# Performance work log

Measured on AMD Instinct MI355X. Metric: run time of the kernel, lower is better.

## Reference

```python
import jax, jax.numpy as jnp
import numpy as np
import math

B, T, XD, H, DD, P = 512, 256, 128, 512, 16, 32
IN = 2 * XD + DD  # GRUCell input size


def _init(key, shape, fan):
    stdv = 1.0 / math.sqrt(fan)
    return jax.random.uniform(key, shape, jnp.float32, -stdv, stdv)


def setup_inputs() -> dict:
    key = jax.random.key(0)
    ks = jax.random.split(key, 32)
    inp = {
        "values": jax.random.normal(ks[0], (B, T, XD), jnp.float32),
        "lens": jnp.full((B,), T, dtype=jnp.int32),  # lens[0] == max_len
        "static": jax.random.normal(ks[1], (B, DD), jnp.float32),
        "times": jax.random.uniform(ks[2], (B, T, XD), jnp.float32),
        "masks": (jax.random.uniform(ks[3], (B, T, XD)) < 0.8).astype(jnp.float32),
        "prototype": jax.random.normal(ks[4], (P, H), jnp.float32),
        "proto": True,
        # temp_decay_h: Linear(x_dim -> hidden), custom uniform(-1/sqrt(H), 1/sqrt(H))
        "Wd": _init(ks[5], (H, XD), H), "bd": _init(ks[6], (H,), XD),
        # hist_reg: Linear(hidden -> x_dim)
        "Wh": _init(ks[7], (XD, H), H), "bh": _init(ks[8], (XD,), H),
        "Wf": _init(ks[9], (XD, XD), XD), "bf": _init(ks[10], (XD,), XD),
        # ProtoAttn Q/K/V: Linear(hidden -> hidden)
        "Wq": _init(ks[11], (H, H), H), "bq": _init(ks[12], (H,), H),
        "Wk": _init(ks[13], (H, H), H), "bk": _init(ks[14], (H,), H),
        "Wv": _init(ks[15], (H, H), H), "bv": _init(ks[16], (H,), H),
        # gating W: Linear(2*hidden -> 1)
        "Wg": _init(ks[17], (1, 2 * H), 2 * H), "bg": _init(ks[18], (1,), 2 * H),
        # GRUCell
        "Wih": _init(ks[19], (3 * H, IN), H), "Whh": _init(ks[20], (3 * H, H), H),
        "bih": _init(ks[21], (3 * H,), H), "bhh": _init(ks[22], (3 * H,), H),
    }
    return inp


def _forward(values, static, times, masks, prototype,
             Wd, bd, Wh, bh, Wf, bf, Wq, bq, Wk, bk, Wv, bv, Wg, bg,
             Wih, Whh, bih, bhh, lens, proto):
    feat_m = 1.0 - jnp.eye(XD, dtype=values.dtype)  # zero-diagonal mask
    gamma = jnp.exp(-jax.nn.relu(jnp.einsum("btx,hx->bth", times, Wd) + bd))
    # attention key/value do not depend on h -> precompute
    keyp = prototype @ Wk.T + bk      # [P,H]
    valp = prototype @ Wv.T + bv      # [P,H]
    scale = 1.0 / math.sqrt(P)
    valid = (jnp.arange(T)[:, None] < lens[None, :]).astype(values.dtype)  # [T,B]

    xs = (jnp.swapaxes(values, 0, 1),  # [T,B,XD]
          jnp.swapaxes(masks, 0, 1),   # [T,B,XD]
          jnp.swapaxes(gamma, 0, 1),   # [T,B,H]
          valid[:, :, None])           # [T,B,1]

    h0 = jnp.zeros((B, H), values.dtype)
    xh0 = jnp.zeros((B, XD), values.dtype)

    def step(carry, xt):
        h, x_h = carry
        x, m, g, v = xt
        if proto:
            q = h @ Wq.T + bq                          # [B,H]
            score = (q @ keyp.T) * scale               # [B,P]
            attn = jax.nn.softmax(score, axis=-1)      # dropout omitted (eval)
            h1 = attn @ valp                           # [B,H]
            alpha = jax.nn.sigmoid(jnp.concatenate([h, h1], axis=1) @ Wg.T + bg)
            h = alpha * h + (1.0 - alpha) * h1
        h = h * g
        x_h = jnp.where(v > 0, h @ Wh.T + bh, x_h)
        x_c = m * x + (1.0 - m) * x_h
        z_h = x_c @ (Wf * feat_m).T + bf
        z_c = m * x + (1.0 - m) * z_h
        inp = jnp.concatenate([z_c, m, static], axis=1)
        gx = inp @ Wih.T + bih
        gh = h @ Whh.T + bhh
        xr, xz, xn = jnp.split(gx, 3, axis=1)
        hr, hz, hn = jnp.split(gh, 3, axis=1)
        r = jax.nn.sigmoid(xr + hr)
        z = jax.nn.sigmoid(xz + hz)
        n = jnp.tanh(xn + r * hn)
        h_new = (1.0 - z) * n + z * h
        h = jnp.where(v > 0, h_new, h)
        return (h, x_h), (h, x_c, z_c)

    (hN, _), (hs, x_cs, z_cs) = jax.lax.scan(step, (h0, xh0), xs)
    hs = jnp.swapaxes(hs, 0, 1)
    x_cs = jnp.swapaxes(x_cs, 0, 1)
    z_cs = jnp.swapaxes(z_cs, 0, 1)
    return hs, hN, x_cs, z_cs


def reference(values, lens, static, times, masks, prototype, proto,
              Wd, bd, Wh, bh, Wf, bf, Wq, bq, Wk, bk, Wv, bv, Wg, bg,
              Wih, Whh, bih, bhh):
    return _forward(values, static, times, masks, prototype,
                    Wd, bd, Wh, bh, Wf, bf, Wq, bq, Wk, bk, Wv, bv, Wg, bg,
                    Wih, Whh, bih, bhh, lens, bool(proto))
```

## Files before the change

kernel.cpp:

```cpp
#include <hip/hip_runtime.h>

#define NB 256
#define NT 1024

#define Bv 512
#define Tv 256
#define XDv 128
#define Hv 512
#define DDv 16
#define Pv 32

typedef short s8 __attribute__((ext_vector_type(8)));
typedef float f4 __attribute__((ext_vector_type(4)));
typedef unsigned long long u64;

#define OFF_KEYP 2048
#define OFF_VALP (OFF_KEYP + 16384)
#define OFF_MF   (OFF_VALP + 16384)
#define OFF_C    (OFF_MF + 16384)
#define OFF_VWG  (OFF_C + 32)
#define OFF_FRG  (OFF_VWG + 32)
#define US_WD   0
#define US_MS   65536
#define US_VP   81920
#define US_WH   98304
#define US_WF   163840
#define US_WHH  180224
#define US_WIH  966656
#define US_END  1409024
#define OFF_H   (OFF_FRG + (US_END/2))

#define OUT_HS  0
#define OUT_HN  (Bv*Tv*Hv)
#define OUT_XCS (OUT_HN + Bv*Hv)
#define OUT_ZCS (OUT_XCS + Bv*Tv*XDv)

struct Smem {
  unsigned short hA[32*520];
  unsigned short tA[32*136];
  unsigned short xcA[32*136];
  unsigned short inpA[32*296];
  unsigned short aA[32*40];
  unsigned short mA[32*136];
  unsigned short xhS[32*128];
  float xvS[32*132];
  float scS[32*34];
  float ghS[3*32*33];
  float gxS[3*32*33];
  float hp32[32*32];
  float al[32], rsm[32], cS[32], vwgS[32];
};

__device__ __forceinline__ unsigned short f2b(float f) {
  union { float f; unsigned int u; } x{f};
  unsigned int r = x.u + 0x7fffu + ((x.u >> 16) & 1u);
  return (unsigned short)(r >> 16);
}
__device__ __forceinline__ float b2f(unsigned short u) {
  union { unsigned int u; float f; } x{(unsigned int)u << 16};
  return x.f;
}
__device__ __forceinline__ float sig_f(float x) { return 1.f / (1.f + __expf(-x)); }
__device__ __forceinline__ float tanh_f(float x) {
  x = fminf(fmaxf(x, -15.f), 15.f);
  float e = __expf(2.f * x);
  return (e - 1.f) / (e + 1.f);
}
__device__ __forceinline__ s8 pack8(const float* p) {
  f4 a = *(const f4*)p; f4 b = *(const f4*)(p + 4);
  s8 r;
  r[0]=(short)f2b(a[0]); r[1]=(short)f2b(a[1]); r[2]=(short)f2b(a[2]); r[3]=(short)f2b(a[3]);
  r[4]=(short)f2b(b[0]); r[5]=(short)f2b(b[1]); r[6]=(short)f2b(b[2]); r[7]=(short)f2b(b[3]);
  return r;
}

__device__ __forceinline__ void gridbar(unsigned int* bar, unsigned int& lgen, int bid) {
  __syncthreads();
  if (threadIdx.x == 0) {
    __threadfence();
    const unsigned int target = ++lgen;
    unsigned int* grp = bar + (bid >> 4)*16;
    const unsigned int a =
        __hip_atomic_fetch_add(grp, 1u, __ATOMIC_ACQ_REL, __HIP_MEMORY_SCOPE_AGENT);
    if (a == 15u) {
      __hip_atomic_store(grp, 0u, __ATOMIC_RELAXED, __HIP_MEMORY_SCOPE_AGENT);
      const unsigned int r =
          __hip_atomic_fetch_add(bar + 384, 1u, __ATOMIC_ACQ_REL, __HIP_MEMORY_SCOPE_AGENT);
      if (r == 15u) {
        __hip_atomic_store(bar + 384, 0u, __ATOMIC_RELAXED, __HIP_MEMORY_SCOPE_AGENT);
        __hip_atomic_store(bar + 400, target, __ATOMIC_RELEASE, __HIP_MEMORY_SCOPE_AGENT);
      }
    }
    while (__hip_atomic_load(bar + 400, __ATOMIC_RELAXED, __HIP_MEMORY_SCOPE_AGENT) < target)
      __builtin_amdgcn_s_sleep(2);
    __threadfence();
  }
  __syncthreads();
}

__device__ __forceinline__ void rgbar_nf(unsigned int* bar, unsigned int& lgen, int rg) {
  __syncthreads();
  if (threadIdx.x == 0) {
    const unsigned int target = ++lgen;
    unsigned int* cnt = bar + 512 + rg*64;
    unsigned int* flg = cnt + 32;
    const unsigned int a =
        __hip_atomic_fetch_add(cnt, 1u, __ATOMIC_RELAXED, __HIP_MEMORY_SCOPE_AGENT);
    if (a == 15u) {
      __hip_atomic_store(cnt, 0u, __ATOMIC_RELAXED, __HIP_MEMORY_SCOPE_AGENT);
      asm volatile("s_waitcnt vmcnt(0)" ::: "memory");
      __hip_atomic_store(flg, target, __ATOMIC_RELAXED, __HIP_MEMORY_SCOPE_AGENT);
    } else {
      while (__hip_atomic_load(flg, __ATOMIC_RELAXED, __HIP_MEMORY_SCOPE_AGENT) < target)
        __builtin_amdgcn_s_sleep(2);
    }
  }
  __syncthreads();
}

#define SWZ(DST, NTILES, KT_, EXPR)                                            \
  { const int tot = (NTILES)*(KT_)*512;                                        \
    for (int f = gtid; f < tot; f += NB*NT) {                                  \
      const int e = f & 7, lane_ = (f >> 3) & 63, rem = f >> 9;                \
      const int kt = rem % (KT_), nt = rem / (KT_);                            \
      const int n = nt*16 + (lane_ & 15);                                      \
      const int k = kt*32 + ((lane_ >> 4) & 3)*8 + e;                          \
      (DST)[f] = f2b((EXPR));                                                  \
    } }

#define MFMA(a,b,c) __builtin_amdgcn_mfma_f32_16x16x32_bf16((a),(b),(c),0,0,0)
#define FRAG(P,idx) (*(const s8*)&(P)[((size_t)(idx))*8])
#define NTST(v,p) __builtin_nontemporal_store((v),(p))

__global__ __launch_bounds__(NT, 4)
void rits_main(const float* __restrict__ values, const int* __restrict__ lens,
               const float* __restrict__ statc, const float* __restrict__ times,
               const float* __restrict__ masks, const float* __restrict__ prototype,
               const int* __restrict__ protoflag,
               const float* __restrict__ Wd, const float* __restrict__ bd,
               const float* __restrict__ Wh, const float* __restrict__ bh,
               const float* __restrict__ Wf, const float* __restrict__ bf,
               const float* __restrict__ Wq, const float* __restrict__ bq,
               const float* __restrict__ Wk, const float* __restrict__ bk,
               const float* __restrict__ Wv, const float* __restrict__ bv,
               const float* __restrict__ Wg, const float* __restrict__ bg,
               const float* __restrict__ Wih, const float* __restrict__ Whh,
               const float* __restrict__ bih, const float* __restrict__ bhh,
               float* __restrict__ out, float* __restrict__ ws)
{
  const int bid = blockIdx.x, tid = threadIdx.x;
  const int gtid = bid*NT + tid;
  const int wv = tid >> 6, ln = tid & 63;
  const int l15 = ln & 15, l4 = ln >> 4;
  const int rg = (bid & 7)*2 + ((bid >> 7) & 1);
  const int cg = (bid >> 3) & 15;
  const int r0 = rg*32, c0 = cg*32;
  unsigned int* bar = (unsigned int*)ws;
  unsigned int lgenG = 0, lgenR = 0;
  unsigned short* frg = (unsigned short*)(ws + OFF_FRG);
  const unsigned short* wdW  = frg + US_WD;
  const unsigned short* msW  = frg + US_MS;
  const unsigned short* vpW  = frg + US_VP;
  const unsigned short* whW  = frg + US_WH;
  const unsigned short* wfW  = frg + US_WF;
  const unsigned short* whhW = frg + US_WHH;
  const unsigned short* wihW = frg + US_WIH;
  unsigned int* wsH = (unsigned int*)(ws + OFF_H);

  __shared__ Smem L;
  const bool proto = protoflag[0] != 0;
  const float scale = 0.17677669529663687f;

  for (int o = gtid; o < 2*Pv*Hv; o += NB*NT) {
    const int which = o >> 14, rem = o & 16383;
    const int p = rem >> 9, j = rem & 511;
    const float* W = which ? Wv : Wk;
    const float* bb = which ? bv : bk;
    const float* pr = prototype + p*Hv;
    const float* wr = W + j*Hv;
    float s = bb[j];
    #pragma unroll 4
    for (int k = 0; k < Hv; ++k) s += pr[k]*wr[k];
    ws[(which ? OFF_VALP : OFF_KEYP) + p*Hv + j] = s;
  }
  SWZ(frg + US_WD, 32, 4,  Wd[n*XDv + k])
  SWZ(frg + US_WH, 8, 16,  Wh[n*Hv + k])
  SWZ(frg + US_WF, 8, 4,   (n == k ? 0.f : Wf[n*XDv + k]))
  SWZ(frg + US_WHH, 96, 16,
      Whh[((size_t)(n >> 9)*Hv + (((n >> 5) & 15)*32 + ((n >> 4) & 1)*16 + (n & 15)))*Hv + k])
  SWZ(frg + US_WIH, 96, 9,
      (k < 272 ? Wih[((size_t)(n >> 9)*Hv + (((n >> 5) & 15)*32 + ((n >> 4) & 1)*16 + (n & 15)))*272 + k] : 0.f))
  gridbar(bar, lgenG, bid);

  {
    const float* keyp = ws + OFF_KEYP;
    const float* valp = ws + OFF_VALP;
    for (int o = gtid; o < Pv*Hv; o += NB*NT) {
      const int p = o >> 9, kc = o & 511;
      float s = 0.f;
      #pragma unroll 4
      for (int j = 0; j < Hv; ++j) s += keyp[p*Hv + j]*Wq[j*Hv + kc];
      ws[OFF_MF + o] = s;
    }
    if (gtid < 32) {
      float s = 0.f;
      for (int j = 0; j < Hv; ++j) s += bq[j]*keyp[gtid*Hv + j];
      ws[OFF_C + gtid] = s;
    } else if (gtid < 64) {
      const int p = gtid - 32;
      float s = 0.f;
      for (int j = 0; j < Hv; ++j) s += valp[p*Hv + j]*Wg[Hv + j];
      ws[OFF_VWG + p] = s;
    }
  }
  gridbar(bar, lgenG, bid);

  SWZ(frg + US_MS, 2, 16, (ws + OFF_MF)[n*Hv + k])
  SWZ(frg + US_VP, 32, 1, (ws + OFF_VALP)[k*Hv + n])
  gridbar(bar, lgenG, bid);

  for (int o = tid; o < 32*128; o += NT) L.xhS[o] = 0;
  if (tid < 32) { L.cS[tid] = ws[OFF_C + tid]; L.vwgS[tid] = ws[OFF_VWG + tid]; }
  for (int o = tid; o < 32*40; o += NT) {
    const int row = o / 40, cc = o % 40;
    L.inpA[row*296 + 256 + cc] =
        (cc < DDv) ? f2b(statc[(r0 + row)*DDv + cc]) : (unsigned short)0;
  }

  const int w8 = wv & 7;
  const int xcol8 = w8*16 + l15;
  const float bhR = bh[xcol8], bfR = bf[xcol8];
  int lensB2[8];
  #pragma unroll
  for (int rt = 0; rt < 2; ++rt)
    #pragma unroll
    for (int i = 0; i < 4; ++i)
      lensB2[rt*4 + i] = lens[r0 + rt*16 + l4*4 + i];
  float wgr[8];
  if (wv >= 8) {
    #pragma unroll
    for (int e = 0; e < 8; ++e) wgr[e] = Wg[ln*8 + e];
  }
  float bdW2[2];
  #pragma unroll
  for (int q = 0; q < 2; ++q) bdW2[q] = bd[(wv*2 + q)*16 + l15];
  const int crow = tid >> 5, cjj = tid & 31;
  float bihR[3], bhhR[3];
  #pragma unroll
  for (int g = 0; g < 3; ++g) { bihR[g] = bih[g*Hv + c0 + cjj]; bhhR[g] = bhh[g*Hv + c0 + cjj]; }
  const int lensG0 = lens[r0 + crow];
  const float bg0 = bg[0];

  float pv[4], pm[4], pt[4];
  #pragma unroll
  for (int i = 0; i < 4; ++i) {
    const int o = i*NT + tid, row = o >> 7, col = o & 127;
    const size_t a = ((size_t)(r0 + row)*Tv + 0)*XDv + col;
    pv[i] = values[a]; pm[i] = masks[a]; pt[i] = times[a];
  }
  __syncthreads();

  for (int t = 0; t < Tv; ++t) {
    if (t > 0) {
      const u64* src64 = (const u64*)(wsH + ((t - 1) & 1)*131072) + (size_t)r0*128;
      #pragma unroll
      for (int i = 0; i < 4; ++i) {
        const int o = i*NT + tid, row = o >> 7, cp = o & 127;
        ((u64*)&L.hA[row*520])[cp] = __hip_atomic_load(
            &src64[(size_t)row*128 + cp], __ATOMIC_RELAXED, __HIP_MEMORY_SCOPE_AGENT);
      }
    } else {
      for (int o = tid; o < 32*128; o += NT) {
        const int row = o >> 7, cp = o & 127;
        ((u64*)&L.hA[row*520])[cp] = 0ull;
      }
    }
    #pragma unroll
    for (int i = 0; i < 4; ++i) {
      const int o = i*NT + tid, row = o >> 7, col = o & 127;
      L.xvS[row*132 + col] = pv[i];
      L.mA[row*136 + col]  = f2b(pm[i]);
      L.tA[row*136 + col]  = f2b(pt[i]);
    }
    {
      const int tn = (t + 1 < Tv) ? t + 1 : t;
      #pragma unroll
      for (int i = 0; i < 4; ++i) {
        const int o = i*NT + tid, row = o >> 7, col = o & 127;
        const size_t a = ((size_t)(r0 + row)*Tv + tn)*XDv + col;
        pv[i] = values[a]; pm[i] = masks[a]; pt[i] = times[a];
      }
    }
    __syncthreads();

    if (proto) {
      if (wv < 2) {
        const int nt = wv;
        f4 acc0 = {0.f,0.f,0.f,0.f}, acc1 = {0.f,0.f,0.f,0.f};
        #pragma unroll
        for (int kt = 0; kt < 16; ++kt) {
          s8 b  = FRAG(msW, (nt*16 + kt)*64 + ln);
          s8 a0 = *(const s8*)&L.hA[(l15)*520 + kt*32 + l4*8];
          s8 a1 = *(const s8*)&L.hA[(16 + l15)*520 + kt*32 + l4*8];
          acc0 = MFMA(a0, b, acc0);
          acc1 = MFMA(a1, b, acc1);
        }
        #pragma unroll
        for (int i = 0; i < 4; ++i) {
          L.scS[(l4*4 + i)*34 + nt*16 + l15]        = acc0[i];
          L.scS[(16 + l4*4 + i)*34 + nt*16 + l15]   = acc1[i];
        }
      } else if (wv >= 8) {
        #pragma unroll
        for (int rr = 0; rr < 4; ++rr) {
          const int row = (wv - 8)*4 + rr;
          s8 hv8 = *(const s8*)&L.hA[row*520 + ln*8];
          float s = 0.f;
          #pragma unroll
          for (int e = 0; e < 8; ++e) s += b2f((unsigned short)hv8[e]) * wgr[e];
          s += __shfl_xor(s, 1);  s += __shfl_xor(s, 2);  s += __shfl_xor(s, 4);
          s += __shfl_xor(s, 8);  s += __shfl_xor(s, 16); s += __shfl_xor(s, 32);
          if (ln == 0) L.scS[row*34 + 32] = s;
        }
      }
    }
    __syncthreads();

    if (proto) {
      const int row = wv*2 + (ln >> 5);
      const int p = ln & 31;
      const float sc = (L.scS[row*34 + p] + L.cS[p]) * scale;
      float mx = sc;
      mx = fmaxf(mx, __shfl_xor(mx, 1));  mx = fmaxf(mx, __shfl_xor(mx, 2));
      mx = fmaxf(mx, __shfl_xor(mx, 4));  mx = fmaxf(mx, __shfl_xor(mx, 8));
      mx = fmaxf(mx, __shfl_xor(mx, 16));
      const float e = __expf(sc - mx);
      float sm = e;
      sm += __shfl_xor(sm, 1); sm += __shfl_xor(sm, 2); sm += __shfl_xor(sm, 4);
      sm += __shfl_xor(sm, 8); sm += __shfl_xor(sm, 16);
      float a1 = e * L.vwgS[p];
      a1 += __shfl_xor(a1, 1); a1 += __shfl_xor(a1, 2); a1 += __shfl_xor(a1, 4);
      a1 += __shfl_xor(a1, 8); a1 += __shfl_xor(a1, 16);
      L.aA[row*40 + p] = f2b(e);
      if (p == 0) {
        L.rsm[row] = 1.f / sm;
        L.al[row] = sig_f(L.scS[row*34 + 32] + a1 / sm + bg0);
      }
    }
    __syncthreads();

    {
      s8 ta[2][4]; s8 aa[2];
      #pragma unroll
      for (int rt = 0; rt < 2; ++rt) {
        #pragma unroll
        for (int kt = 0; kt < 4; ++kt)
          ta[rt][kt] = *(const s8*)&L.tA[(rt*16 + l15)*136 + kt*32 + l4*8];
        if (proto) aa[rt] = *(const s8*)&L.aA[(rt*16 + l15)*40 + l4*8];
      }
      #pragma unroll
      for (int q = 0; q < 2; ++q) {
        const int nt = wv*2 + q;
        const int col = nt*16 + l15;
        f4 g2[2] = {{0.f,0.f,0.f,0.f},{0.f,0.f,0.f,0.f}};
        f4 h12[2] = {{0.f,0.f,0.f,0.f},{0.f,0.f,0.f,0.f}};
        #pragma unroll
        for (int kt = 0; kt < 4; ++kt) {
          s8 b = FRAG(wdW, (nt*4 + kt)*64 + ln);
          g2[0] = MFMA(ta[0][kt], b, g2[0]);
          g2[1] = MFMA(ta[1][kt], b, g2[1]);
        }
        if (proto) {
          s8 b = FRAG(vpW, nt*64 + ln);
          h12[0] = MFMA(aa[0], b, h12[0]);
          h12[1] = MFMA(aa[1], b, h12[1]);
        }
        #pragma unroll
        for (int rt = 0; rt < 2; ++rt) {
          #pragma unroll
          for (int i = 0; i < 4; ++i) {
            const int row = rt*16 + l4*4 + i;
            const float gam = __expf(-fmaxf(g2[rt][i] + bdW2[q], 0.f));
            const float hbf = b2f(L.hA[row*520 + col]);
            float hp;
            if (proto) {
              const float av = L.al[row];
              hp = (av*hbf + (1.f - av)*h12[rt][i]*L.rsm[row]) * gam;
            } else hp = hbf * gam;
            L.hA[row*520 + col] = f2b(hp);
            const unsigned cc = (unsigned)(col - c0);
            if (cc < 32u) L.hp32[row*32 + cc] = hp;
          }
        }
      }
    }
    __syncthreads();

    if (wv < 8) {
      f4 accX[2] = {{0.f,0.f,0.f,0.f},{0.f,0.f,0.f,0.f}};
      #pragma unroll
      for (int kt = 0; kt < 16; ++kt) {
        s8 b  = FRAG(whW, (wv*16 + kt)*64 + ln);
        s8 a0 = *(const s8*)&L.hA[(l15)*520 + kt*32 + l4*8];
        s8 a1 = *(const s8*)&L.hA[(16 + l15)*520 + kt*32 + l4*8];
        accX[0] = MFMA(a0, b, accX[0]);
        accX[1] = MFMA(a1, b, accX[1]);
      }
      #pragma unroll
      for (int rt = 0; rt < 2; ++rt) {
        #pragma unroll
        for (int i = 0; i < 4; ++i) {
          const int row = rt*16 + l4*4 + i;
          const int b = r0 + row;
          float xh = accX[rt][i] + bhR;
          if (t < lensB2[rt*4 + i]) L.xhS[row*128 + xcol8] = f2b(xh);
          else                      xh = b2f(L.xhS[row*128 + xcol8]);
          const float xv = L.xvS[row*132 + xcol8], mv = b2f(L.mA[row*136 + xcol8]);
          const float xc = mv*xv + (1.f - mv)*xh;
          if (cg == 0) NTST(xc, &out[OUT_XCS + ((size_t)b*Tv + t)*XDv + xcol8]);
          L.xcA[row*136 + xcol8] = f2b(xc);
        }
      }
    } else if (wv < 14) {
      const int j = wv - 8, g = j >> 1, hf = j & 1;
      const int ntG = g*32 + cg*2 + hf;
      const int cLoc = hf*16 + l15;
      f4 accG[2] = {{0.f,0.f,0.f,0.f},{0.f,0.f,0.f,0.f}};
      #pragma unroll
      for (int kt = 0; kt < 16; ++kt) {
        s8 b  = FRAG(whhW, (ntG*16 + kt)*64 + ln);
        s8 a0 = *(const s8*)&L.hA[(l15)*520 + kt*32 + l4*8];
        s8 a1 = *(const s8*)&L.hA[(16 + l15)*520 + kt*32 + l4*8];
        accG[0] = MFMA(a0, b, accG[0]);
        accG[1] = MFMA(a1, b, accG[1]);
      }
      #pragma unroll
      for (int rt = 0; rt < 2; ++rt)
        #pragma unroll
        for (int i = 0; i < 4; ++i)
          L.ghS[g*1056 + (rt*16 + l4*4 + i)*33 + cLoc] = accG[rt][i];
    }
    __syncthreads();

    {
      const int wrt = wv >> 3;
      f4 acc = {0.f,0.f,0.f,0.f};
      #pragma unroll
      for (int kt = 0; kt < 4; ++kt) {
        s8 a = *(const s8*)&L.xcA[(wrt*16 + l15)*136 + kt*32 + l4*8];
        acc = MFMA(a, FRAG(wfW, (w8*4 + kt)*64 + ln), acc);
      }
      #pragma unroll
      for (int i = 0; i < 4; ++i) {
        const int row = wrt*16 + l4*4 + i;
        const float xv = L.xvS[row*132 + xcol8], mv = b2f(L.mA[row*136 + xcol8]);
        const float zc = mv*xv + (1.f - mv)*(acc[i] + bfR);
        if (cg == 0) NTST(zc, &out[OUT_ZCS + ((size_t)(r0 + row)*Tv + t)*XDv + xcol8]);
        L.inpA[row*296 + xcol8]       = f2b(zc);
        L.inpA[row*296 + 128 + xcol8] = f2b(mv);
      }
    }
    __syncthreads();

    if (wv < 12) {
      const int g = wv >> 2, sub = wv & 3;
      const int hf = sub >> 1, rt = sub & 1;
      const int ntG = g*32 + cg*2 + hf;
      const int cLoc = hf*16 + l15;
      f4 acc = {0.f,0.f,0.f,0.f};
      #pragma unroll
      for (int kt = 0; kt < 9; ++kt) {
        s8 a = *(const s8*)&L.inpA[(rt*16 + l15)*296 + kt*32 + l4*8];
        acc = MFMA(a, FRAG(wihW, (ntG*9 + kt)*64 + ln), acc);
      }
      #pragma unroll
      for (int i = 0; i < 4; ++i)
        L.gxS[g*1056 + (rt*16 + l4*4 + i)*33 + cLoc] = acc[i];
    }
    __syncthreads();

    unsigned int* dst = wsH + (t & 1)*131072;
    {
      const int row = crow;
      const int b = r0 + row, jc = c0 + cjj;
      const float xr = L.gxS[row*33 + cjj]        + bihR[0];
      const float xz = L.gxS[1056 + row*33 + cjj] + bihR[1];
      const float xn = L.gxS[2112 + row*33 + cjj] + bihR[2];
      const float hr = L.ghS[row*33 + cjj]        + bhhR[0];
      const float hz = L.ghS[1056 + row*33 + cjj] + bhhR[1];
      const float hn = L.ghS[2112 + row*33 + cjj] + bhhR[2];
      const float r = sig_f(xr + hr), z = sig_f(xz + hz);
      const float n = tanh_f(xn + r*hn);
      const float hpv = L.hp32[row*32 + cjj];
      const float hfv = (t < lensG0) ? ((1.f - z)*n + z*hpv) : hpv;
      NTST(hfv, &out[OUT_HS + ((size_t)b*Tv + t)*Hv + jc]);
      if (t == Tv - 1) NTST(hfv, &out[OUT_HN + (size_t)b*Hv + jc]);
      const float partner = __shfl_xor(hfv, 1);
      if ((cjj & 1) == 0) {
        const unsigned int pk = (unsigned int)f2b(hfv) | ((unsigned int)f2b(partner) << 16);
        __hip_atomic_store(&dst[(size_t)b*256 + cg*16 + (cjj >> 1)], pk,
                           __ATOMIC_RELAXED, __HIP_MEMORY_SCOPE_AGENT);
      }
    }
    rgbar_nf(bar, lgenR, rg);
  }
}

extern "C" void kernel_launch(void* const* d_in, const int* in_sizes, int n_in,
                              void* d_out, int out_size, void* d_ws, size_t ws_size,
                              hipStream_t stream) {
  (void)in_sizes; (void)n_in; (void)out_size; (void)ws_size;
  hipMemsetAsync(d_ws, 0, 8192, stream);
  rits_main<<<NB, NT, 0, stream>>>(
      (const float*)d_in[0],  (const int*)d_in[1],   (const float*)d_in[2],
      (const float*)d_in[3],  (const float*)d_in[4], (const float*)d_in[5],
      (const int*)d_in[6],
      (const float*)d_in[7],  (const float*)d_in[8],
      (const float*)d_in[9],  (const float*)d_in[10],
      (const float*)d_in[11], (const float*)d_in[12],
      (const float*)d_in[13], (const float*)d_in[14],
      (const float*)d_in[15], (const float*)d_in[16],
      (const float*)d_in[17], (const float*)d_in[18],
      (const float*)d_in[19], (const float*)d_in[20],
      (const float*)d_in[21], (const float*)d_in[22],
      (const float*)d_in[23], (const float*)d_in[24],
      (float*)d_out, (float*)d_ws);
}
```

Before: 14.38 ms.

## Preload MFMA weight fragments into registers and rebalance per-wave roles

Each wave now loads its Wh/Whh/proto-score B fragments and its Wf fragments into registers once, before the time loop, instead of re-reading them from LDS/global every step. The prototype-score MFMA moves to waves 14-15 and the gating dot product moves to waves 0-7, so the two proto tasks run on otherwise idle waves. The x_c/z_c output stores are spread across column groups instead of all going through cg==0. This raises register pressure considerably (20 s8 fragments per lane), which risks spills or lower occupancy.

```diff
diff --git a/kernel.cpp b/kernel.cpp
--- a/kernel.cpp
+++ b/kernel.cpp
@@ -228,8 +228,31 @@
   }
 
   const int w8 = wv & 7;
+  s8 fB2[16];
+  if (wv < 8) {
+    #pragma unroll
+    for (int kt = 0; kt < 16; ++kt)
+      fB2[kt] = FRAG(whW, (wv*16 + kt)*64 + ln);
+  } else if (wv < 14) {
+    const int j = wv - 8, g = j >> 1, hf = j & 1;
+    const int ntG = g*32 + cg*2 + hf;
+    #pragma unroll
+    for (int kt = 0; kt < 16; ++kt)
+      fB2[kt] = FRAG(whhW, (ntG*16 + kt)*64 + ln);
+  } else {
+    const int nt = wv - 14;
+    #pragma unroll
+    for (int kt = 0; kt < 16; ++kt)
+      fB2[kt] = FRAG(msW, (nt*16 + kt)*64 + ln);
+  }
+  s8 fB3[4];
+  #pragma unroll
+  for (int kt = 0; kt < 4; ++kt)
+    fB3[kt] = FRAG(wfW, (w8*4 + kt)*64 + ln);
+
   const int xcol8 = w8*16 + l15;
   const float bhR = bh[xcol8], bfR = bf[xcol8];
+  const int wcg = xcol8 >> 3;
   int lensB2[8];
   #pragma unroll
   for (int rt = 0; rt < 2; ++rt)
@@ -237,7 +260,7 @@
     for (int i = 0; i < 4; ++i)
       lensB2[rt*4 + i] = lens[r0 + rt*16 + l4*4 + i];
   float wgr[8];
-  if (wv >= 8) {
+  if (wv < 8) {
     #pragma unroll
     for (int e = 0; e < 8; ++e) wgr[e] = Wg[ln*8 + e];
   }
@@ -294,26 +317,25 @@
     __syncthreads();
 
     if (proto) {
-      if (wv < 2) {
-        const int nt = wv;
+      if (wv >= 14) {
+        const int nt = wv - 14;
         f4 acc0 = {0.f,0.f,0.f,0.f}, acc1 = {0.f,0.f,0.f,0.f};
         #pragma unroll
         for (int kt = 0; kt < 16; ++kt) {
-          s8 b  = FRAG(msW, (nt*16 + kt)*64 + ln);
           s8 a0 = *(const s8*)&L.hA[(l15)*520 + kt*32 + l4*8];
           s8 a1 = *(const s8*)&L.hA[(16 + l15)*520 + kt*32 + l4*8];
-          acc0 = MFMA(a0, b, acc0);
-          acc1 = MFMA(a1, b, acc1);
+          acc0 = MFMA(a0, fB2[kt], acc0);
+          acc1 = MFMA(a1, fB2[kt], acc1);
         }
         #pragma unroll
         for (int i = 0; i < 4; ++i) {
-          L.scS[(l4*4 + i)*34 + nt*16 + l15]        = acc0[i];
-          L.scS[(16 + l4*4 + i)*34 + nt*16 + l15]   = acc1[i];
-        }
-      } else if (wv >= 8) {
+          L.scS[(l4*4 + i)*34 + nt*16 + l15]      = acc0[i];
+          L.scS[(16 + l4*4 + i)*34 + nt*16 + l15] = acc1[i];
+        }
+      } else if (wv < 8) {
         #pragma unroll
         for (int rr = 0; rr < 4; ++rr) {
-          const int row = (wv - 8)*4 + rr;
+          const int row = wv*4 + rr;
           s8 hv8 = *(const s8*)&L.hA[row*520 + ln*8];
           float s = 0.f;
           #pragma unroll
@@ -400,11 +422,10 @@
       f4 accX[2] = {{0.f,0.f,0.f,0.f},{0.f,0.f,0.f,0.f}};
       #pragma unroll
       for (int kt = 0; kt < 16; ++kt) {
-        s8 b  = FRAG(whW, (wv*16 + kt)*64 + ln);
         s8 a0 = *(const s8*)&L.hA[(l15)*520 + kt*32 + l4*8];
         s8 a1 = *(const s8*)&L.hA[(16 + l15)*520 + kt*32 + l4*8];
-        accX[0] = MFMA(a0, b, accX[0]);
-        accX[1] = MFMA(a1, b, accX[1]);
+        accX[0] = MFMA(a0, fB2[kt], accX[0]);
+        accX[1] = MFMA(a1, fB2[kt], accX[1]);
       }
       #pragma unroll
       for (int rt = 0; rt < 2; ++rt) {
@@ -417,22 +438,20 @@
           else                      xh = b2f(L.xhS[row*128 + xcol8]);
           const float xv = L.xvS[row*132 + xcol8], mv = b2f(L.mA[row*136 + xcol8]);
           const float xc = mv*xv + (1.f - mv)*xh;
-          if (cg == 0) NTST(xc, &out[OUT_XCS + ((size_t)b*Tv + t)*XDv + xcol8]);
+          if (wcg == cg) NTST(xc, &out[OUT_XCS + ((size_t)b*Tv + t)*XDv + xcol8]);
           L.xcA[row*136 + xcol8] = f2b(xc);
         }
       }
     } else if (wv < 14) {
       const int j = wv - 8, g = j >> 1, hf = j & 1;
-      const int ntG = g*32 + cg*2 + hf;
       const int cLoc = hf*16 + l15;
       f4 accG[2] = {{0.f,0.f,0.f,0.f},{0.f,0.f,0.f,0.f}};
       #pragma unroll
       for (int kt = 0; kt < 16; ++kt) {
-        s8 b  = FRAG(whhW, (ntG*16 + kt)*64 + ln);
         s8 a0 = *(const s8*)&L.hA[(l15)*520 + kt*32 + l4*8];
         s8 a1 = *(const s8*)&L.hA[(16 + l15)*520 + kt*32 + l4*8];
-        accG[0] = MFMA(a0, b, accG[0]);
-        accG[1] = MFMA(a1, b, accG[1]);
+        accG[0] = MFMA(a0, fB2[kt], accG[0]);
+        accG[1] = MFMA(a1, fB2[kt], accG[1]);
       }
       #pragma unroll
       for (int rt = 0; rt < 2; ++rt)
@@ -448,14 +467,14 @@
       #pragma unroll
       for (int kt = 0; kt < 4; ++kt) {
         s8 a = *(const s8*)&L.xcA[(wrt*16 + l15)*136 + kt*32 + l4*8];
-        acc = MFMA(a, FRAG(wfW, (w8*4 + kt)*64 + ln), acc);
+        acc = MFMA(a, fB3[kt], acc);
       }
       #pragma unroll
       for (int i = 0; i < 4; ++i) {
         const int row = wrt*16 + l4*4 + i;
         const float xv = L.xvS[row*132 + xcol8], mv = b2f(L.mA[row*136 + xcol8]);
         const float zc = mv*xv + (1.f - mv)*(acc[i] + bfR);
-        if (cg == 0) NTST(zc, &out[OUT_ZCS + ((size_t)(r0 + row)*Tv + t)*XDv + xcol8]);
+        if (wcg == cg) NTST(zc, &out[OUT_ZCS + ((size_t)(r0 + row)*Tv + t)*XDv + xcol8]);
         L.inpA[row*296 + xcol8]       = f2b(zc);
         L.inpA[row*296 + 128 + xcol8] = f2b(mv);
       }
```

After: 17.83 ms. 24.0% more time.
